# Performance work log

Hardware: AMD Instinct MI355X
Metric: run time of the kernel (lower is better)

## Reference

```python
import jax, jax.numpy as jnp
import numpy as np
from jax import lax

NUM_HEADS = 4
EPS = 1e-12  # torch F.normalize eps


def _dwconv3(x, w):
    # depthwise 3x3 conv, padding 1; w: (C,1,3,3)
    return lax.conv_general_dilated(
        x, w, window_strides=(1, 1), padding=((1, 1), (1, 1)),
        dimension_numbers=('NCHW', 'OIHW', 'NCHW'),
        feature_group_count=w.shape[0])


def _make_qkv(x, w_qkv, w_dw):
    # 1x1 conv (GEMM over channels) then depthwise 3x3
    y = jnp.einsum('bchw,oc->bohw', x, w_qkv)
    y = _dwconv3(y, w_dw)
    b, c3, h, w = y.shape
    c = c3 // 3
    q, k, v = jnp.split(y, 3, axis=1)
    rs = lambda t: t.reshape(b, NUM_HEADS, c // NUM_HEADS, h * w)
    return rs(q), rs(k), rs(v)


def _l2norm(t):
    # F.normalize(t, dim=-1): t / max(||t||_2, eps)
    n = jnp.sqrt(jnp.sum(t * t, axis=-1, keepdims=True))
    return t / jnp.maximum(n, EPS)


def _attend(q, k, v, temperature):
    # channel-wise attention: scores are (b, h, d, d)
    scores = jnp.einsum('bhdn,bhen->bhde', q, k) * temperature
    attn = jax.nn.softmax(scores, axis=-1)
    return jnp.einsum('bhde,bhen->bhdn', attn, v), attn


def setup_inputs() -> dict:
    key = jax.random.key(0)
    ks = jax.random.split(key, 8)
    B, C, H, W = 4, 192, 128, 128
    C3 = 3 * C
    return {
        'e': jax.random.normal(ks[0], (B, C, H, W), jnp.float32),
        'd': jax.random.normal(ks[1], (B, C, H, W), jnp.float32),
        'temperature': jnp.ones((1, NUM_HEADS, 1, 1), jnp.float32),
        'w_qkv': jax.random.normal(ks[2], (C3, C), jnp.float32) * 0.05,
        'w_dw': jax.random.normal(ks[3], (C3, 1, 3, 3), jnp.float32) * 0.1,
        'w_p1': jax.random.normal(ks[4], (C, C), jnp.float32) * 0.05,
        'w_p2': jax.random.normal(ks[5], (C, C), jnp.float32) * 0.05,
        'w_p3': jax.random.normal(ks[6], (C, C), jnp.float32) * 0.05,
        'w_p4': jax.random.normal(ks[7], (C, C), jnp.float32) * 0.05,
    }


def reference(e, d, temperature, w_qkv, w_dw, w_p1, w_p2, w_p3, w_p4):
    b, c, h, w = e.shape
    q_e, k_e, v_e = _make_qkv(e, w_qkv, w_dw)
    q_d, k_d, v_d = _make_qkv(d, w_qkv, w_dw)
    q_e, k_e = _l2norm(q_e), _l2norm(k_e)
    q_d, k_d = _l2norm(q_d), _l2norm(k_d)

    proj = lambda o, wp: jnp.einsum('bchw,oc->bohw', o.reshape(b, c, h, w), wp)

    out_ee, _ = _attend(q_e, k_e, v_e, temperature)
    out_dd, _ = _attend(q_d, k_d, v_d, temperature)
    intra_e = proj(out_ee, w_p1)
    intra_d = proj(out_dd, w_p2)

    out_ed, _ = _attend(q_e, k_d, v_d, temperature)
    # cross d->e: replicate torch's squeeze(0) (no-op unless b==1)
    scores_de = jnp.einsum('bhdn,bhen->bhde', q_d, k_e) * temperature
    attn_de = jax.nn.softmax(scores_de, axis=-1)
    if attn_de.shape[0] == 1:
        attn_de = attn_de[0]
    out_de = jnp.einsum('...de,bhen->bhdn', attn_de, v_e)
    inter_ed = proj(out_ed, w_p3)
    inter_de = proj(out_de, w_p4)
    return (intra_e, intra_d, inter_ed, inter_de)
```

## Files before the change

### kernel.cpp

```cpp
#include <hip/hip_runtime.h>

#define N_PIX 16384
#define CC 192
#define C3 576
#define KTOT 192
#define NCH 32
#define CHUNK 512
#define WTILE 12800

typedef __bf16 bf16_t;
typedef bf16_t bf16x4 __attribute__((ext_vector_type(4)));
typedef bf16_t bf16x8 __attribute__((ext_vector_type(8)));
typedef float f32x4 __attribute__((ext_vector_type(4)));

struct WPtrs { const float* p[4]; };
struct GArgs { long xoff[16]; long yoff[16]; long woff[16]; int sel[16]; };

template <typename XT, typename YT, int NC, int NMT>
__global__ __launch_bounds__(256) void gemm_mloop(GArgs ga,
    const XT* __restrict__ X0, const XT* __restrict__ X1,
    YT* __restrict__ Y, const bf16_t* __restrict__ Wpad)
{
    __shared__ __align__(16) bf16_t Wl[2][WTILE];
    __shared__ __align__(16) char Ustage[17408];
    const int z = blockIdx.y;
    const XT* __restrict__ Xb = (ga.sel[z] ? X1 : X0) + ga.xoff[z];
    const int n0 = blockIdx.x * 128;
    const int tid = threadIdx.x;
    const int w = tid >> 6;
    const int gi = (tid >> 4) & 3;
    const int li = tid & 15;

    bf16x8 xfrag[6][2];
    {
        XT* stg = (XT*)Ustage;
        const int kr = tid >> 3;
        const int nq = tid & 7;
        for (int kc = 0; kc < 6; ++kc) {
            const XT* xp = Xb + (long)(32 * kc + kr) * N_PIX + n0 + 16 * nq;
            XT* sp = stg + kr * 136 + 16 * nq;
            if constexpr (sizeof(XT) == 4) {
                f32x4 a = *(const f32x4*)(xp);
                f32x4 b = *(const f32x4*)(xp + 4);
                f32x4 c = *(const f32x4*)(xp + 8);
                f32x4 d4 = *(const f32x4*)(xp + 12);
                *(f32x4*)(sp) = a;   *(f32x4*)(sp + 4) = b;
                *(f32x4*)(sp + 8) = c; *(f32x4*)(sp + 12) = d4;
            } else {
                bf16x8 a = *(const bf16x8*)(xp);
                bf16x8 b = *(const bf16x8*)(xp + 8);
                *(bf16x8*)(sp) = a;  *(bf16x8*)(sp + 8) = b;
            }
            __syncthreads();
            #pragma unroll
            for (int ni = 0; ni < 2; ++ni) {
                const int nn = 32 * w + 16 * ni + li;
                bf16x8 v;
                #pragma unroll
                for (int e = 0; e < 8; ++e)
                    v[e] = (bf16_t)stg[(8 * gi + e) * 136 + nn];
                xfrag[kc][ni] = v;
            }
            __syncthreads();
        }
    }

    auto dmaW = [&](int it, int buf) {
        const int c = it / NMT, j = it % NMT;
        const char* src = (const char*)(Wpad + ga.woff[z * NC + c]
                                        + (long)j * WTILE);
        char* dst = (char*)&Wl[buf][0];
        #pragma unroll
        for (int r = 0; r < 6; ++r)
            __builtin_amdgcn_global_load_lds(
                (const __attribute__((address_space(1))) void*)
                    (src + r * 4096 + tid * 16),
                (__attribute__((address_space(3))) void*)
                    (dst + r * 4096 + w * 1024),
                16, 0, 0);
        if (w == 0)
            __builtin_amdgcn_global_load_lds(
                (const __attribute__((address_space(1))) void*)
                    (src + 24576 + tid * 16),
                (__attribute__((address_space(3))) void*)(dst + 24576),
                16, 0, 0);
    };

    dmaW(0, 0);
    __syncthreads();

    for (int it = 0; it < NC * NMT; ++it) {
        const int cur = it & 1;
        if (it + 1 < NC * NMT) dmaW(it + 1, cur ^ 1);
        f32x4 acc[4][2];
        #pragma unroll
        for (int i = 0; i < 4; ++i)
            #pragma unroll
            for (int jj = 0; jj < 2; ++jj) acc[i][jj] = 0.f;
        #pragma unroll
        for (int t = 0; t < 6; ++t) {
            bf16x8 af[4];
            #pragma unroll
            for (int mi = 0; mi < 4; ++mi)
                af[mi] = *(const bf16x8*)
                    &Wl[cur][(16 * mi + li) * 200 + 32 * t + 8 * gi];
            #pragma unroll
            for (int mi = 0; mi < 4; ++mi)
                #pragma unroll
                for (int ni = 0; ni < 2; ++ni)
                    acc[mi][ni] = __builtin_amdgcn_mfma_f32_16x16x32_bf16(
                        xfrag[t][ni], af[mi], acc[mi][ni], 0, 0, 0);
        }
        const int c = it / NMT, j = it % NMT;
        if constexpr (sizeof(YT) == 2) {
            bf16_t* et = (bf16_t*)Ustage;
            #pragma unroll
            for (int mi = 0; mi < 4; ++mi)
                #pragma unroll
                for (int ni = 0; ni < 2; ++ni) {
                    bf16x4 v = { (bf16_t)acc[mi][ni][0], (bf16_t)acc[mi][ni][1],
                                 (bf16_t)acc[mi][ni][2], (bf16_t)acc[mi][ni][3] };
                    *(bf16x4*)&et[(16 * mi + li) * 136
                                  + 32 * w + 16 * ni + 4 * gi] = v;
                }
            __syncthreads();
            YT* Yb = Y + ga.yoff[z * NC + c] + (long)(64 * j) * N_PIX + n0;
            const int r0 = tid >> 4, p = tid & 15;
            #pragma unroll
            for (int j4 = 0; j4 < 4; ++j4) {
                const int row = r0 + 16 * j4;
                bf16x8 v = *(const bf16x8*)&et[row * 136 + 8 * p];
                *(bf16x8*)(Yb + (long)row * N_PIX + 8 * p) = v;
            }
        } else {
            YT* Yb = Y + ga.yoff[z * NC + c] + (long)(64 * j) * N_PIX;
            #pragma unroll
            for (int mi = 0; mi < 4; ++mi)
                #pragma unroll
                for (int ni = 0; ni < 2; ++ni) {
                    YT* yp = Yb + (long)(16 * mi + li) * N_PIX
                               + n0 + 32 * w + 16 * ni + 4 * gi;
                    *(f32x4*)yp = acc[mi][ni];
                }
        }
        __syncthreads();
    }
}

__global__ __launch_bounds__(256) void prep_w(const float* __restrict__ wq,
                                              bf16_t* __restrict__ wpad)
{
    const int j = blockIdx.x, tid = threadIdx.x;
    for (int idx = tid; idx < 64 * 192; idx += 256) {
        const int r = idx / 192, c = idx - r * 192;
        wpad[(long)j * WTILE + r * 200 + c] =
            (bf16_t)wq[(long)(64 * j + r) * KTOT + c];
    }
}

__global__ __launch_bounds__(256) void dwconv3b(const bf16_t* __restrict__ Yin,
    const float* __restrict__ wdw, bf16_t* __restrict__ Z,
    float* __restrict__ invn)
{
    const int ch = blockIdx.x, sb = blockIdx.y;
    const int tid = threadIdx.x;
    const int x0 = (tid & 15) << 3;
    const int y0 = (tid >> 4) << 3;
    const bf16_t* __restrict__ inp = Yin + (long)(sb * C3 + ch) * N_PIX;
    bf16_t* __restrict__ outp = Z + (long)(sb * C3 + ch) * N_PIX;
    const float* wch = wdw + ch * 9;
    const float w00 = wch[0], w01 = wch[1], w02 = wch[2];
    const float w10 = wch[3], w11 = wch[4], w12 = wch[5];
    const float w20 = wch[6], w21 = wch[7], w22 = wch[8];
    const bool hasL = (x0 > 0), hasR = (x0 < 120);
    float A[10], B[10], Cr[10];
    auto loadrow = [&](int yy, float* r) {
        if (yy < 0 || yy > 127) {
            #pragma unroll
            for (int i = 0; i < 10; ++i) r[i] = 0.f;
            return;
        }
        const bf16_t* p = inp + (yy << 7);
        bf16x8 v = *(const bf16x8*)(p + x0);
        #pragma unroll
        for (int j = 0; j < 8; ++j) r[1 + j] = (float)v[j];
        r[0] = hasL ? (float)p[x0 - 1] : 0.f;
        r[9] = hasR ? (float)p[x0 + 8] : 0.f;
    };
    loadrow(y0 - 1, A);
    loadrow(y0,     B);
    float ss = 0.f;
    #pragma unroll
    for (int r = 0; r < 8; ++r) {
        loadrow(y0 + r + 1, Cr);
        bf16x8 ov;
        #pragma unroll
        for (int i = 0; i < 8; ++i) {
            float s;
            s = fmaf(w00, A[i],  fmaf(w01, A[i + 1],  w02 * A[i + 2]));
            s = fmaf(w10, B[i],  fmaf(w11, B[i + 1],  fmaf(w12, B[i + 2], s)));
            s = fmaf(w20, Cr[i], fmaf(w21, Cr[i + 1], fmaf(w22, Cr[i + 2], s)));
            ov[i] = (bf16_t)s;
            const float vb = (float)ov[i];
            ss = fmaf(vb, vb, ss);
        }
        *(bf16x8*)(outp + ((y0 + r) << 7) + x0) = ov;
        #pragma unroll
        for (int i = 0; i < 10; ++i) { A[i] = B[i]; B[i] = Cr[i]; }
    }
    if (ch < 384) {
        #pragma unroll
        for (int off = 32; off > 0; off >>= 1) ss += __shfl_down(ss, off);
        __shared__ float red[4];
        if ((tid & 63) == 0) red[tid >> 6] = ss;
        __syncthreads();
        if (tid == 0) {
            const float t = red[0] + red[1] + red[2] + red[3];
            const int row = (sb >> 2) * 1536 + (sb & 3) * 384 + ch;
            invn[row] = 1.f / fmaxf(sqrtf(t), 1e-12f);
        }
    }
}

__global__ __launch_bounds__(256) void scores_mfma(const bf16_t* __restrict__ Z,
                                                   float* __restrict__ part)
{
    const int c = blockIdx.x;
    const int bh = blockIdx.y;
    const int b = bh >> 2, h = bh & 3;
    __shared__ __align__(16) bf16_t T[4][48][72];
    const int tid = threadIdx.x;
    const int m = tid >> 6;
    const int gi = (tid >> 4) & 3, li = tid & 15;
    const int qs = (m == 1 || m == 3) ? 1 : 0;
    const int ks = (m == 1 || m == 2) ? 1 : 0;
    f32x4 acc[3][3];
    #pragma unroll
    for (int i = 0; i < 3; ++i)
        #pragma unroll
        for (int j = 0; j < 3; ++j) acc[i][j] = 0.f;

    const int nbase = c * CHUNK;
    for (int k0 = 0; k0 < CHUNK; k0 += 64) {
        __syncthreads();
        for (int l = tid; l < 1536; l += 256) {
            const int t = l / 384;
            const int rem = l - t * 384;
            const int r = rem >> 3, s = rem & 7;
            const int sidx = (t < 2) ? t : (t - 2);
            const int qk = (t < 2) ? 0 : 1;
            const bf16_t* gp = Z + ((long)((sidx * 4 + b) * C3 + qk * 192 + h * 48 + r)) * N_PIX
                                 + nbase + k0 + s * 8;
            *(bf16x8*)&T[t][r][s * 8] = *(const bf16x8*)gp;
        }
        __syncthreads();
        #pragma unroll
        for (int k2 = 0; k2 < 64; k2 += 32) {
            bf16x8 af[3], bfr[3];
            #pragma unroll
            for (int i = 0; i < 3; ++i) {
                bf16x4 lo = *(const bf16x4*)&T[qs][16 * i + li][k2 + 4 * gi];
                bf16x4 hi = *(const bf16x4*)&T[qs][16 * i + li][k2 + 16 + 4 * gi];
                af[i] = __builtin_shufflevector(lo, hi, 0, 1, 2, 3, 4, 5, 6, 7);
            }
            #pragma unroll
            for (int j = 0; j < 3; ++j) {
                bf16x4 lo = *(const bf16x4*)&T[2 + ks][16 * j + li][k2 + 4 * gi];
                bf16x4 hi = *(const bf16x4*)&T[2 + ks][16 * j + li][k2 + 16 + 4 * gi];
                bfr[j] = __builtin_shufflevector(lo, hi, 0, 1, 2, 3, 4, 5, 6, 7);
            }
            #pragma unroll
            for (int i = 0; i < 3; ++i)
                #pragma unroll
                for (int j = 0; j < 3; ++j)
                    acc[i][j] = __builtin_amdgcn_mfma_f32_16x16x32_bf16(
                        af[i], bfr[j], acc[i][j], 0, 0, 0);
        }
    }
    const long base = ((long)(m * 16 + bh) * NCH + c) * 2304;
    #pragma unroll
    for (int i = 0; i < 3; ++i)
        #pragma unroll
        for (int j = 0; j < 3; ++j) {
            const int e = 16 * j + li;
            #pragma unroll
            for (int r = 0; r < 4; ++r) {
                const int d = 16 * i + 4 * gi + r;
                part[base + d * 48 + e] = acc[i][j][r];
            }
        }
}

__global__ __launch_bounds__(256) void reduce_softmax(const float* __restrict__ part,
    const float* __restrict__ invn, const float* __restrict__ temp,
    float* __restrict__ attn)
{
    const int mbh = blockIdx.x;
    const int m = mbh >> 4, b = (mbh >> 2) & 3, h = mbh & 3;
    const int qs = (m == 1 || m == 3) ? 1 : 0;
    const int ks = (m == 1 || m == 2) ? 1 : 0;
    __shared__ float sm[48][48];
    const int tid = threadIdx.x;
    const long pbase = (long)mbh * NCH * 2304;
    const float T = temp[h];
    for (int idx = tid; idx < 2304; idx += 256) {
        float v = 0.f;
        #pragma unroll 8
        for (int c = 0; c < NCH; ++c) v += part[pbase + c * 2304 + idx];
        const int d = idx / 48, e = idx % 48;
        const float iq = invn[(qs * 4 + b) * 384 + h * 48 + d];
        const float ik = invn[(ks * 4 + b) * 384 + 192 + h * 48 + e];
        sm[d][e] = v * iq * ik * T;
    }
    __syncthreads();
    if (tid < 48) {
        float mx = -1e30f;
        #pragma unroll
        for (int e = 0; e < 48; ++e) mx = fmaxf(mx, sm[tid][e]);
        float sum = 0.f;
        #pragma unroll
        for (int e = 0; e < 48; ++e) {
            const float v = __expf(sm[tid][e] - mx);
            sm[tid][e] = v;
            sum += v;
        }
        const float inv = 1.f / sum;
        const long abase = (long)mbh * 2304 + (long)tid * 48;
        #pragma unroll
        for (int e = 0; e < 48; ++e) attn[abase + e] = sm[tid][e] * inv;
    }
}

__global__ __launch_bounds__(256) void make_M(const float* __restrict__ attn,
                                              WPtrs wp, bf16_t* __restrict__ Mpad)
{
    const int h = blockIdx.x & 3;
    const int b = (blockIdx.x >> 2) & 3;
    const int m = blockIdx.x >> 4;
    __shared__ float A[48][48];
    const int tid = threadIdx.x;
    if (m == 3) {
        for (int l = tid; l < 2304; l += 256) {
            float s = 0.f;
            #pragma unroll
            for (int bb = 0; bb < 16; ++bb)
                s += attn[(long)(48 + bb) * 2304 + l];
            A[l / 48][l % 48] = s;
        }
    } else {
        const long ab = (long)(m * 16 + b * 4 + h) * 2304;
        for (int l = tid; l < 2304; l += 256)
            A[l / 48][l % 48] = attn[ab + l];
    }
    __syncthreads();
    const float* W = wp.p[m];
    bf16_t* Mo = Mpad + (long)(m * 4 + b) * 3 * WTILE;
    for (int o = tid >> 4; o < 192; o += 16) {
        const float* wrow = W + (long)o * 192 + h * 48;
        bf16_t* orow = Mo + (long)(o >> 6) * WTILE + (o & 63) * 200 + h * 48;
        for (int e2 = tid & 15; e2 < 48; e2 += 16) {
            float s = 0.f;
            #pragma unroll
            for (int d = 0; d < 48; ++d) s = fmaf(wrow[d], A[d][e2], s);
            orow[e2] = (bf16_t)s;
        }
    }
}

extern "C" void kernel_launch(void* const* d_in, const int* in_sizes, int n_in,
                              void* d_out, int out_size, void* d_ws, size_t ws_size,
                              hipStream_t stream)
{
    const float* e     = (const float*)d_in[0];
    const float* d     = (const float*)d_in[1];
    const float* temp  = (const float*)d_in[2];
    const float* w_qkv = (const float*)d_in[3];
    const float* w_dw  = (const float*)d_in[4];
    const float* w_p1  = (const float*)d_in[5];
    const float* w_p2  = (const float*)d_in[6];
    const float* w_p3  = (const float*)d_in[7];
    const float* w_p4  = (const float*)d_in[8];
    float* out = (float*)d_out;
    float* ws  = (float*)d_ws;

    bf16_t* zraw = (bf16_t*)ws;
    bf16_t* zb   = (bf16_t*)(ws + 37748736L);
    float* attn  = ws + 75497472L;
    float* invn  = ws + 75644928L;
    bf16_t* Wqpad = (bf16_t*)(ws + 75648000L);
    bf16_t* Mpad  = (bf16_t*)(ws + 75710000L);
    float* part  = ws;

    const long sXin = (long)CC * N_PIX;
    const long sQKV = (long)C3 * N_PIX;

    prep_w<<<dim3(9), 256, 0, stream>>>(w_qkv, Wqpad);
    GArgs gq{};
    for (int z = 0; z < 8; ++z) {
        gq.xoff[z] = (long)(z & 3) * sXin;
        gq.yoff[z] = (long)z * sQKV;
        gq.woff[z] = 0;
        gq.sel[z] = z >> 2;
    }
    gemm_mloop<float, bf16_t, 1, 9><<<dim3(128, 8), 256, 0, stream>>>(
        gq, e, d, zraw, Wqpad);
    dwconv3b<<<dim3(C3, 8), 256, 0, stream>>>(zraw, w_dw, zb, invn);
    scores_mfma<<<dim3(NCH, 16), 256, 0, stream>>>(zb, part);
    reduce_softmax<<<dim3(64), 256, 0, stream>>>(part, invn, temp, attn);
    WPtrs wpj; wpj.p[0] = w_p1; wpj.p[1] = w_p2; wpj.p[2] = w_p3; wpj.p[3] = w_p4;
    make_M<<<dim3(64), 256, 0, stream>>>(attn, wpj, Mpad);
    GArgs gm{};
    for (int z = 0; z < 8; ++z) {
        const int s = z >> 2, b = z & 3;
        gm.xoff[z] = ((long)((s * 4 + b) * C3 + 384)) * N_PIX;
        gm.sel[z] = 0;
        for (int c = 0; c < 2; ++c) {
            const int midx = (s == 0) ? (c ? 3 : 0) : (c ? 2 : 1);
            gm.woff[2 * z + c] = (long)(midx * 4 + b) * 3 * WTILE;
            gm.yoff[2 * z + c] = (long)(midx * 4 + b) * sXin;
        }
    }
    gemm_mloop<bf16_t, float, 2, 3><<<dim3(128, 8), 256, 0, stream>>>(
        gm, zb, zb, out, Mpad);
}
```

Before: 304.3 us.

## Halve GEMM shared memory: single-buffer weight tile and split staging passes

After: 309.3 us. No clear change (+1.6%).

```diff
diff --git a/kernel.cpp b/kernel.cpp
--- a/kernel.cpp
+++ b/kernel.cpp
@@ -21,8 +21,8 @@
     const XT* __restrict__ X0, const XT* __restrict__ X1,
     YT* __restrict__ Y, const bf16_t* __restrict__ Wpad)
 {
-    __shared__ __align__(16) bf16_t Wl[2][WTILE];
-    __shared__ __align__(16) char Ustage[17408];
+    __shared__ __align__(16) bf16_t Wl[WTILE];
+    __shared__ __align__(16) char Ustage[8704];
     const int z = blockIdx.y;
     const XT* __restrict__ Xb = (ga.sel[z] ? X1 : X0) + ga.xoff[z];
     const int n0 = blockIdx.x * 128;
@@ -31,45 +31,11 @@
     const int gi = (tid >> 4) & 3;
     const int li = tid & 15;
 
-    bf16x8 xfrag[6][2];
-    {
-        XT* stg = (XT*)Ustage;
-        const int kr = tid >> 3;
-        const int nq = tid & 7;
-        for (int kc = 0; kc < 6; ++kc) {
-            const XT* xp = Xb + (long)(32 * kc + kr) * N_PIX + n0 + 16 * nq;
-            XT* sp = stg + kr * 136 + 16 * nq;
-            if constexpr (sizeof(XT) == 4) {
-                f32x4 a = *(const f32x4*)(xp);
-                f32x4 b = *(const f32x4*)(xp + 4);
-                f32x4 c = *(const f32x4*)(xp + 8);
-                f32x4 d4 = *(const f32x4*)(xp + 12);
-                *(f32x4*)(sp) = a;   *(f32x4*)(sp + 4) = b;
-                *(f32x4*)(sp + 8) = c; *(f32x4*)(sp + 12) = d4;
-            } else {
-                bf16x8 a = *(const bf16x8*)(xp);
-                bf16x8 b = *(const bf16x8*)(xp + 8);
-                *(bf16x8*)(sp) = a;  *(bf16x8*)(sp + 8) = b;
-            }
-            __syncthreads();
-            #pragma unroll
-            for (int ni = 0; ni < 2; ++ni) {
-                const int nn = 32 * w + 16 * ni + li;
-                bf16x8 v;
-                #pragma unroll
-                for (int e = 0; e < 8; ++e)
-                    v[e] = (bf16_t)stg[(8 * gi + e) * 136 + nn];
-                xfrag[kc][ni] = v;
-            }
-            __syncthreads();
-        }
-    }
-
-    auto dmaW = [&](int it, int buf) {
+    auto dmaW = [&](int it) {
         const int c = it / NMT, j = it % NMT;
         const char* src = (const char*)(Wpad + ga.woff[z * NC + c]
                                         + (long)j * WTILE);
-        char* dst = (char*)&Wl[buf][0];
+        char* dst = (char*)&Wl[0];
         #pragma unroll
         for (int r = 0; r < 6; ++r)
             __builtin_amdgcn_global_load_lds(
@@ -86,12 +52,58 @@
                 16, 0, 0);
     };
 
-    dmaW(0, 0);
-    __syncthreads();
+    dmaW(0);
+
+    bf16x8 xfrag[6][2];
+    if constexpr (sizeof(XT) == 4) {
+        float* stg = (float*)Ustage;
+        const int kr = tid >> 4;
+        const int nq = tid & 15;
+        for (int kc = 0; kc < 12; ++kc) {
+            const int t = kc >> 1, kh = kc & 1;
+            const XT* xp = Xb + (long)(32 * t + 16 * kh + kr) * N_PIX
+                              + n0 + 8 * nq;
+            float* sp = stg + kr * 136 + 8 * nq;
+            *(f32x4*)(sp)     = *(const f32x4*)(xp);
+            *(f32x4*)(sp + 4) = *(const f32x4*)(xp + 4);
+            __syncthreads();
+            if ((gi >> 1) == kh) {
+                #pragma unroll
+                for (int ni = 0; ni < 2; ++ni) {
+                    const int nn = 32 * w + 16 * ni + li;
+                    bf16x8 v;
+                    #pragma unroll
+                    for (int e = 0; e < 8; ++e)
+                        v[e] = (bf16_t)stg[(8 * (gi & 1) + e) * 136 + nn];
+                    xfrag[t][ni] = v;
+                }
+            }
+            __syncthreads();
+        }
+    } else {
+        bf16_t* stg = (bf16_t*)Ustage;
+        const int kr = tid >> 3;
+        const int nq = tid & 7;
+        for (int kc = 0; kc < 6; ++kc) {
+            const XT* xp = Xb + (long)(32 * kc + kr) * N_PIX + n0 + 16 * nq;
+            bf16_t* sp = stg + kr * 136 + 16 * nq;
+            *(bf16x8*)(sp)     = *(const bf16x8*)(xp);
+            *(bf16x8*)(sp + 8) = *(const bf16x8*)(xp + 8);
+            __syncthreads();
+            #pragma unroll
+            for (int ni = 0; ni < 2; ++ni) {
+                const int nn = 32 * w + 16 * ni + li;
+                bf16x8 v;
+                #pragma unroll
+                for (int e = 0; e < 8; ++e)
+                    v[e] = stg[(8 * gi + e) * 136 + nn];
+                xfrag[kc][ni] = v;
+            }
+            __syncthreads();
+        }
+    }
 
     for (int it = 0; it < NC * NMT; ++it) {
-        const int cur = it & 1;
-        if (it + 1 < NC * NMT) dmaW(it + 1, cur ^ 1);
         f32x4 acc[4][2];
         #pragma unroll
         for (int i = 0; i < 4; ++i)
@@ -103,7 +115,7 @@
             #pragma unroll
             for (int mi = 0; mi < 4; ++mi)
                 af[mi] = *(const bf16x8*)
-                    &Wl[cur][(16 * mi + li) * 200 + 32 * t + 8 * gi];
+                    &Wl[(16 * mi + li) * 200 + 32 * t + 8 * gi];
             #pragma unroll
             for (int mi = 0; mi < 4; ++mi)
                 #pragma unroll
@@ -114,25 +126,39 @@
         const int c = it / NMT, j = it % NMT;
         if constexpr (sizeof(YT) == 2) {
             bf16_t* et = (bf16_t*)Ustage;
-            #pragma unroll
-            for (int mi = 0; mi < 4; ++mi)
-                #pragma unroll
-                for (int ni = 0; ni < 2; ++ni) {
-                    bf16x4 v = { (bf16_t)acc[mi][ni][0], (bf16_t)acc[mi][ni][1],
-                                 (bf16_t)acc[mi][ni][2], (bf16_t)acc[mi][ni][3] };
-                    *(bf16x4*)&et[(16 * mi + li) * 136
-                                  + 32 * w + 16 * ni + 4 * gi] = v;
+            YT* Yb = Y + ga.yoff[z * NC + c] + (long)(64 * j) * N_PIX + n0;
+            #pragma unroll
+            for (int p = 0; p < 2; ++p) {
+                #pragma unroll
+                for (int mh = 0; mh < 2; ++mh) {
+                    const int mi = 2 * p + mh;
+                    #pragma unroll
+                    for (int ni = 0; ni < 2; ++ni) {
+                        bf16x4 v = { (bf16_t)acc[mi][ni][0],
+                                     (bf16_t)acc[mi][ni][1],
+                                     (bf16_t)acc[mi][ni][2],
+                                     (bf16_t)acc[mi][ni][3] };
+                        *(bf16x4*)&et[(16 * mh + li) * 136
+                                      + 32 * w + 16 * ni + 4 * gi] = v;
+                    }
                 }
-            __syncthreads();
-            YT* Yb = Y + ga.yoff[z * NC + c] + (long)(64 * j) * N_PIX + n0;
-            const int r0 = tid >> 4, p = tid & 15;
-            #pragma unroll
-            for (int j4 = 0; j4 < 4; ++j4) {
-                const int row = r0 + 16 * j4;
-                bf16x8 v = *(const bf16x8*)&et[row * 136 + 8 * p];
-                *(bf16x8*)(Yb + (long)row * N_PIX + 8 * p) = v;
+                __syncthreads();
+                if (p == 0 && it + 1 < NC * NMT)
+                    dmaW(it + 1);
+                {
+                    const int lr = tid >> 4, pc = tid & 15;
+                    #pragma unroll
+                    for (int j4 = 0; j4 < 2; ++j4) {
+                        const int row = lr + 16 * j4;
+                        bf16x8 v = *(const bf16x8*)&et[row * 136 + 8 * pc];
+                        *(bf16x8*)(Yb + (long)(32 * p + row) * N_PIX + 8 * pc) = v;
+                    }
+                }
+                __syncthreads();
             }
         } else {
+            __syncthreads();
+            if (it + 1 < NC * NMT) dmaW(it + 1);
             YT* Yb = Y + ga.yoff[z * NC + c] + (long)(64 * j) * N_PIX;
             #pragma unroll
             for (int mi = 0; mi < 4; ++mi)
@@ -142,8 +168,8 @@
                                + n0 + 32 * w + 16 * ni + 4 * gi;
                     *(f32x4*)yp = acc[mi][ni];
                 }
-        }
-        __syncthreads();
+            __syncthreads();
+        }
     }
 }
 
```
